# Performance work log

Hardware: AMD Instinct MI355X
Metric: run time of the kernel (lower is better)

Reference implementation:

```python
import jax, jax.numpy as jnp
import numpy as np

T, B, D, O = 2048, 32, 512, 512


def setup_inputs() -> dict:
    key = jax.random.key(0)
    ks = jax.random.split(key, 12)
    s = 0.02
    return {
        "word": jax.random.normal(ks[0], (T, B, D), dtype=jnp.float32),
        "Wf": jax.random.normal(ks[1], (D, D), dtype=jnp.float32) * s,
        "bf": jax.random.normal(ks[2], (D,), dtype=jnp.float32) * s,
        "Wi": jax.random.normal(ks[3], (D, D), dtype=jnp.float32) * s,
        "bi": jax.random.normal(ks[4], (D,), dtype=jnp.float32) * s,
        "Wz": jax.random.normal(ks[5], (D, D), dtype=jnp.float32) * s,
        "bz": jax.random.normal(ks[6], (D,), dtype=jnp.float32) * s,
        "Wo": jax.random.normal(ks[7], (D, D), dtype=jnp.float32) * s,
        "bo": jax.random.normal(ks[8], (D,), dtype=jnp.float32) * s,
        "Wy": jax.random.normal(ks[9], (O, D), dtype=jnp.float32) * s,
        "by": jax.random.normal(ks[10], (O,), dtype=jnp.float32) * s,
    }


def reference(word, Wf, bf, Wi, bi, Wz, bz, Wo, bo, Wy, by):
    # Faithful to the original buggy module:
    #  - forward discards the updated cell state, so c == 0 every step and
    #    the zf gate (wf) never affects the output.
    #  - z and zo reuse wi(hidden) instead of wz/wo(hidden).
    #  - the same Linear is applied to letter and hidden, so bias is doubled
    #    in zi (and zf).
    Bsz, Dd = word.shape[1], word.shape[2]

    def step(h, x):  # h: [B, D], x: [B, D]
        hWi = h @ Wi.T                                  # reused by zi, z, zo
        zi = jax.nn.sigmoid(x @ Wi.T + hWi + 2.0 * bi)
        z = jax.nn.sigmoid(x @ Wz.T + bz + hWi + bi)
        zo = jax.nn.sigmoid(x @ Wo.T + bo + hWi + bi)
        c = zi * z                                      # zf * 0 + zi * z
        h_new = zo * jnp.tanh(c)
        return h_new, None

    h0 = jnp.zeros((Bsz, Dd), dtype=word.dtype)
    h_final, _ = jax.lax.scan(step, h0, word)
    # original computes wy(hidden) every step but only returns the last one
    output = h_final @ Wy.T + by                        # [B, O]
    return output
```

## Files before the change

kernel.cpp:

```cpp
#include <hip/hip_runtime.h>

typedef unsigned int u32;
typedef unsigned short u16;
typedef unsigned long long u64;
typedef _Float16 f16;
typedef f16 f16x2 __attribute__((ext_vector_type(2)));

__device__ __forceinline__ float fdot2(u32 a, u32 b, float c) {
#if __has_builtin(__builtin_amdgcn_fdot2)
    return __builtin_amdgcn_fdot2(__builtin_bit_cast(f16x2, a),
                                  __builtin_bit_cast(f16x2, b), c, false);
#else
    f16x2 av = __builtin_bit_cast(f16x2, a), bv = __builtin_bit_cast(f16x2, b);
    c += (float)av[0] * (float)bv[0];
    c += (float)av[1] * (float)bv[1];
    return c;
#endif
}

__device__ __forceinline__ u32 pack2h(float a, float b) {
    f16x2 h; h[0] = (f16)a; h[1] = (f16)b;
    return __builtin_bit_cast(u32, h);
}
__device__ __forceinline__ float h2f(u16 x) { return (float)__builtin_bit_cast(f16, x); }
__device__ __forceinline__ u16 f2h(float x) { f16 h = (f16)x; return __builtin_bit_cast(u16, h); }

__device__ __forceinline__ float fexp(float x) {
#if __has_builtin(__builtin_amdgcn_exp2f)
    return __builtin_amdgcn_exp2f(x * 1.44269504088896f);
#else
    return __expf(x);
#endif
}
__device__ __forceinline__ float frcp(float x) {
#if __has_builtin(__builtin_amdgcn_rcpf)
    return __builtin_amdgcn_rcpf(x);
#else
    return 1.0f / x;
#endif
}
__device__ __forceinline__ float fsigmoid(float x) { return frcp(1.0f + fexp(-x)); }
__device__ __forceinline__ float ftanh_pos(float x) { return 1.0f - 2.0f * frcp(fexp(2.0f * x) + 1.0f); }

__global__ __launch_bounds__(256) void k0_pack(const float* __restrict__ Wi,
                                               const float* __restrict__ Wy,
                                               u32* __restrict__ WpkT,
                                               u32* __restrict__ Wypk) {
    const int bx = blockIdx.x, tid = threadIdx.x;
    if (bx < 512) {
        const float2 v = *(const float2*)(Wi + (size_t)bx * 512 + 2 * tid);
        WpkT[(size_t)bx * 256 + tid] = pack2h(v.x, v.y);
    } else {
        const int p = bx - 512;
        #pragma unroll
        for (int r = 0; r < 2; ++r) {
            const int d = tid + 256 * r;
            Wypk[(size_t)p * 512 + d] =
                pack2h(Wy[(size_t)d * 512 + 2 * p], Wy[(size_t)d * 512 + 2 * p + 1]);
        }
    }
}

__global__ __launch_bounds__(256) void k1_gates(
    const float* __restrict__ word,
    const float* __restrict__ Wi, const float* __restrict__ Wz, const float* __restrict__ Wo,
    const float* __restrict__ bi, const float* __restrict__ bz, const float* __restrict__ bo,
    u16* __restrict__ Xi, u16* __restrict__ Xz, u16* __restrict__ Xo)
{
    __shared__ uint4 ws2v[3][128][4];
    __shared__ u32 xs2[2][16][36];

    const int tid = threadIdx.x;
    const int d_l = tid & 63;
    const int bq  = tid >> 6;
    const int t0  = blockIdx.x * 2;
    const int d0  = blockIdx.y * 128;

    const float* Wg[3] = {Wi, Wz, Wo};

    float acc[2][2][8][3];
    #pragma unroll
    for (int tt = 0; tt < 2; ++tt)
        #pragma unroll
        for (int db = 0; db < 2; ++db)
            #pragma unroll
            for (int j = 0; j < 8; ++j)
                #pragma unroll
                for (int g = 0; g < 3; ++g) acc[tt][db][j][g] = 0.0f;

    for (int k0c = 0; k0c < 512; k0c += 32) {
        {
            const int p = tid & 15, bg = tid >> 4;
            #pragma unroll
            for (int tt = 0; tt < 2; ++tt)
                #pragma unroll
                for (int j = 0; j < 2; ++j) {
                    const int bb = bg * 2 + j;
                    const float2 v = *(const float2*)(word + (((size_t)(t0 + tt) * 32 + bb) * 512 + k0c + 2 * p));
                    xs2[tt][p][bb] = pack2h(v.x, v.y);
                }
        }
        {
            #pragma unroll
            for (int cc = 0; cc < 6; ++cc) {
                const int c = tid + 256 * cc;
                const int g = c >> 9, r = c & 511, pg = r >> 7, i = r & 127;
                const float* src = Wg[g] + (size_t)(d0 + i) * 512 + k0c + 8 * pg;
                const float4 v0 = ((const float4*)src)[0];
                const float4 v1 = ((const float4*)src)[1];
                uint4 cell;
                cell.x = pack2h(v0.x, v0.y); cell.y = pack2h(v0.z, v0.w);
                cell.z = pack2h(v1.x, v1.y); cell.w = pack2h(v1.z, v1.w);
                ws2v[g][i][(pg + (i >> 2)) & 3] = cell;
            }
        }
        __syncthreads();
        #pragma unroll
        for (int pg = 0; pg < 4; ++pg) {
            uint4 wc[3][2];
            #pragma unroll
            for (int g = 0; g < 3; ++g)
                #pragma unroll
                for (int db = 0; db < 2; ++db) {
                    const int d = d_l + 64 * db;
                    wc[g][db] = ws2v[g][d][(pg + (d >> 2)) & 3];
                }
            #pragma unroll
            for (int p = 0; p < 4; ++p) {
                const int pair = 4 * pg + p;
                u32 x2[2][8];
                #pragma unroll
                for (int tt = 0; tt < 2; ++tt) {
                    const uint4* xr = (const uint4*)&xs2[tt][pair][bq * 8];
                    uint4 xa = xr[0], xb = xr[1];
                    x2[tt][0] = xa.x; x2[tt][1] = xa.y; x2[tt][2] = xa.z; x2[tt][3] = xa.w;
                    x2[tt][4] = xb.x; x2[tt][5] = xb.y; x2[tt][6] = xb.z; x2[tt][7] = xb.w;
                }
                u32 w[3][2];
                #pragma unroll
                for (int g = 0; g < 3; ++g)
                    #pragma unroll
                    for (int db = 0; db < 2; ++db) {
                        const uint4 v = wc[g][db];
                        w[g][db] = (p == 0) ? v.x : (p == 1) ? v.y : (p == 2) ? v.z : v.w;
                    }
                #pragma unroll
                for (int tt = 0; tt < 2; ++tt)
                    #pragma unroll
                    for (int db = 0; db < 2; ++db)
                        #pragma unroll
                        for (int j = 0; j < 8; ++j)
                            #pragma unroll
                            for (int g = 0; g < 3; ++g)
                                acc[tt][db][j][g] = fdot2(x2[tt][j], w[g][db], acc[tt][db][j][g]);
            }
        }
        __syncthreads();
    }

    #pragma unroll
    for (int db = 0; db < 2; ++db) {
        const int d = d0 + 64 * db + d_l;
        const float b0 = 2.0f * bi[d];
        const float b1 = bz[d] + bi[d];
        const float b2 = bo[d] + bi[d];
        #pragma unroll
        for (int tt = 0; tt < 2; ++tt)
            #pragma unroll
            for (int j = 0; j < 8; ++j) {
                const size_t o = ((size_t)(t0 + tt) * 32 + (bq * 8 + j)) * 512 + d;
                Xi[o] = f2h(acc[tt][db][j][0] + b0);
                Xz[o] = f2h(acc[tt][db][j][1] + b1);
                Xo[o] = f2h(acc[tt][db][j][2] + b2);
            }
    }
}

__global__ __launch_bounds__(512, 1) void k2_recur(
    const u16* __restrict__ Xi, const u16* __restrict__ Xz, const u16* __restrict__ Xo,
    const u32* __restrict__ WpkT, const u32* __restrict__ Wypk,
    u64* __restrict__ exch,
    const float* __restrict__ by, float* __restrict__ out)
{
    __shared__ alignas(16) u16 hb[2][256];
    __shared__ alignas(16) u16 hfull[512];

    const int bid  = blockIdx.x;
    const int b    = bid >> 1;
    const int half = bid & 1;
    const int tid  = threadIdx.x;

    const uint4* WpkT4 = (const uint4*)WpkT;
    uint4 w[32];
    #pragma unroll
    for (int i = 0; i < 32; ++i) w[i] = WpkT4[(size_t)tid * 64 + half * 32 + i];

    if (tid < 256) hb[0][tid] = (u16)0;
    __syncthreads();

    u64* eo = exch + ((size_t)(b * 2 + half) * 2) * 512 + tid;
    const u64* ei = exch + ((size_t)(b * 2 + (half ^ 1)) * 2) * 512 + tid;

    const int ownhalf = ((tid >> 8) == half);
    const int hloc = tid & 255;

    u16 xi_c = Xi[(size_t)b * 512 + tid];
    u16 xz_c = Xz[(size_t)b * 512 + tid];
    u16 xo_c = Xo[(size_t)b * 512 + tid];

    float hn = 0.0f;
    for (int t = 0; t < 2048; ++t) {
        const int par = t & 1;
        const int tn = (t + 1) & 2047;
        const size_t xb = ((size_t)tn * 32 + b) * 512 + tid;
        const u16 xi_n = Xi[xb], xz_n = Xz[xb], xo_n = Xo[xb];

        const uint4* hv = (const uint4*)&hb[par][0];
        float a0 = 0.f, a1 = 0.f, a2 = 0.f, a3 = 0.f;
        #pragma unroll
        for (int i = 0; i < 32; ++i) {
            const uint4 hc = hv[i];
            a0 = fdot2(hc.x, w[i].x, a0);
            a1 = fdot2(hc.y, w[i].y, a1);
            a2 = fdot2(hc.z, w[i].z, a2);
            a3 = fdot2(hc.w, w[i].w, a3);
        }
        const float p = (a0 + a1) + (a2 + a3);

        const u64 msg = ((u64)(u32)(t + 1) << 32) | (u64)__builtin_bit_cast(u32, p);
        __hip_atomic_store(eo + (size_t)par * 512, msg,
                           __ATOMIC_RELAXED, __HIP_MEMORY_SCOPE_AGENT);
        u64 m;
        do {
            m = __hip_atomic_load(ei + (size_t)par * 512,
                                  __ATOMIC_RELAXED, __HIP_MEMORY_SCOPE_AGENT);
        } while ((u32)(m >> 32) != (u32)(t + 1));
        const float v = p + __builtin_bit_cast(float, (u32)m);

        const float zi = fsigmoid(h2f(xi_c) + v);
        const float z  = fsigmoid(h2f(xz_c) + v);
        const float zo = fsigmoid(h2f(xo_c) + v);
        hn = zo * ftanh_pos(zi * z);

        if (ownhalf) hb[par ^ 1][hloc] = f2h(hn);
        __syncthreads();

        xi_c = xi_n; xz_c = xz_n; xo_c = xo_n;
    }

    hfull[tid] = f2h(hn);
    __syncthreads();
    {
        const uint4* hv = (const uint4*)&hfull[0];
        float e0 = 0.f, e1 = 0.f, e2 = 0.f, e3 = 0.f;
        #pragma unroll 8
        for (int i = 0; i < 64; ++i) {
            const uint4 hc = hv[i];
            e0 = fdot2(hc.x, Wypk[(size_t)(4 * i + 0) * 512 + tid], e0);
            e1 = fdot2(hc.y, Wypk[(size_t)(4 * i + 1) * 512 + tid], e1);
            e2 = fdot2(hc.z, Wypk[(size_t)(4 * i + 2) * 512 + tid], e2);
            e3 = fdot2(hc.w, Wypk[(size_t)(4 * i + 3) * 512 + tid], e3);
        }
        out[(size_t)b * 512 + tid] = (e0 + e1) + (e2 + e3) + by[tid];
    }
}

extern "C" void kernel_launch(void* const* d_in, const int* in_sizes, int n_in,
                              void* d_out, int out_size, void* d_ws, size_t ws_size,
                              hipStream_t stream) {
    const float* word = (const float*)d_in[0];
    const float* Wi = (const float*)d_in[3];
    const float* bi = (const float*)d_in[4];
    const float* Wz = (const float*)d_in[5];
    const float* bz = (const float*)d_in[6];
    const float* Wo = (const float*)d_in[7];
    const float* bo = (const float*)d_in[8];
    const float* Wy = (const float*)d_in[9];
    const float* by = (const float*)d_in[10];
    float* out = (float*)d_out;

    char* ws = (char*)d_ws;
    const size_t XN = (size_t)2048 * 32 * 512 * sizeof(u16);
    u16* Xi = (u16*)(ws);
    u16* Xz = (u16*)(ws + XN);
    u16* Xo = (u16*)(ws + 2 * XN);
    u32* WpkT = (u32*)(ws + 3 * XN);
    u32* Wypk = (u32*)(ws + 3 * XN + (size_t)524288);
    u64* exch = (u64*)(ws + 3 * XN + (size_t)2 * 524288);

    k0_pack<<<768, 256, 0, stream>>>(Wi, Wy, WpkT, Wypk);

    dim3 g1(1024, 4);
    k1_gates<<<g1, 256, 0, stream>>>(word, Wi, Wz, Wo, bi, bz, bo, Xi, Xz, Xo);

    k2_recur<<<64, 512, 0, stream>>>(Xi, Xz, Xo, WpkT, Wypk, exch, by, out);
}
```

Before: 4.449 ms.

## Exchange partial sums via dual L2/agent channels and remap block pairing

```diff
diff --git a/kernel.cpp b/kernel.cpp
--- a/kernel.cpp
+++ b/kernel.cpp
@@ -41,6 +41,16 @@
 }
 __device__ __forceinline__ float fsigmoid(float x) { return frcp(1.0f + fexp(-x)); }
 __device__ __forceinline__ float ftanh_pos(float x) { return 1.0f - 2.0f * frcp(fexp(2.0f * x) + 1.0f); }
+
+__device__ __forceinline__ u64 load_l2(const u64* p) {
+    u64 v;
+    asm volatile("global_load_dwordx2 %0, %1, off sc0\n\ts_waitcnt vmcnt(0)"
+                 : "=v"(v) : "v"(p) : "memory");
+    return v;
+}
+__device__ __forceinline__ void store_l2(u64* p, u64 v) {
+    asm volatile("global_store_dwordx2 %0, %1, off sc0" :: "v"(p), "v"(v) : "memory");
+}
 
 __global__ __launch_bounds__(256) void k0_pack(const float* __restrict__ Wi,
                                                const float* __restrict__ Wy,
@@ -176,30 +186,38 @@
     }
 }
 
-__global__ __launch_bounds__(512, 1) void k2_recur(
+__global__ __launch_bounds__(512, 2) void k2_recur(
     const u16* __restrict__ Xi, const u16* __restrict__ Xz, const u16* __restrict__ Xo,
     const u32* __restrict__ WpkT, const u32* __restrict__ Wypk,
-    u64* __restrict__ exch,
+    u64* __restrict__ exchF, u64* __restrict__ exchS,
     const float* __restrict__ by, float* __restrict__ out)
 {
     __shared__ alignas(16) u16 hb[2][256];
     __shared__ alignas(16) u16 hfull[512];
 
     const int bid  = blockIdx.x;
-    const int b    = bid >> 1;
-    const int half = bid & 1;
+    const int half = (bid >> 3) & 1;
+    const int b    = (bid & 7) | ((bid >> 4) << 3);
     const int tid  = threadIdx.x;
 
     const uint4* WpkT4 = (const uint4*)WpkT;
-    uint4 w[32];
+    u32 wq[128];
     #pragma unroll
-    for (int i = 0; i < 32; ++i) w[i] = WpkT4[(size_t)tid * 64 + half * 32 + i];
+    for (int i = 0; i < 32; ++i) {
+        const uint4 v = WpkT4[(size_t)tid * 64 + half * 32 + i];
+        wq[4 * i + 0] = v.x; wq[4 * i + 1] = v.y;
+        wq[4 * i + 2] = v.z; wq[4 * i + 3] = v.w;
+    }
+    #pragma unroll
+    for (int i = 0; i < 128; ++i) asm volatile("" : "+v"(wq[i]));
 
     if (tid < 256) hb[0][tid] = (u16)0;
     __syncthreads();
 
-    u64* eo = exch + ((size_t)(b * 2 + half) * 2) * 512 + tid;
-    const u64* ei = exch + ((size_t)(b * 2 + (half ^ 1)) * 2) * 512 + tid;
+    const size_t me  = (size_t)(b * 2 + half) * 2 * 512 + tid;
+    const size_t pa  = (size_t)(b * 2 + (half ^ 1)) * 2 * 512 + tid;
+    u64* eoF = exchF + me;  u64* eoS = exchS + me;
+    const u64* eiF = exchF + pa;  const u64* eiS = exchS + pa;
 
     const int ownhalf = ((tid >> 8) == half);
     const int hloc = tid & 255;
@@ -220,21 +238,27 @@
         #pragma unroll
         for (int i = 0; i < 32; ++i) {
             const uint4 hc = hv[i];
-            a0 = fdot2(hc.x, w[i].x, a0);
-            a1 = fdot2(hc.y, w[i].y, a1);
-            a2 = fdot2(hc.z, w[i].z, a2);
-            a3 = fdot2(hc.w, w[i].w, a3);
+            a0 = fdot2(hc.x, wq[4 * i + 0], a0);
+            a1 = fdot2(hc.y, wq[4 * i + 1], a1);
+            a2 = fdot2(hc.z, wq[4 * i + 2], a2);
+            a3 = fdot2(hc.w, wq[4 * i + 3], a3);
         }
         const float p = (a0 + a1) + (a2 + a3);
 
-        const u64 msg = ((u64)(u32)(t + 1) << 32) | (u64)__builtin_bit_cast(u32, p);
-        __hip_atomic_store(eo + (size_t)par * 512, msg,
+        const u32 tag = (u32)(t + 1);
+        const u64 msg = ((u64)tag << 32) | (u64)__builtin_bit_cast(u32, p);
+        store_l2(eoF + (size_t)par * 512, msg);
+        __hip_atomic_store(eoS + (size_t)par * 512, msg,
                            __ATOMIC_RELAXED, __HIP_MEMORY_SCOPE_AGENT);
+
         u64 m;
-        do {
-            m = __hip_atomic_load(ei + (size_t)par * 512,
+        for (;;) {
+            m = load_l2(eiF + (size_t)par * 512);
+            if ((u32)(m >> 32) == tag) break;
+            m = __hip_atomic_load(eiS + (size_t)par * 512,
                                   __ATOMIC_RELAXED, __HIP_MEMORY_SCOPE_AGENT);
-        } while ((u32)(m >> 32) != (u32)(t + 1));
+            if ((u32)(m >> 32) == tag) break;
+        }
         const float v = p + __builtin_bit_cast(float, (u32)m);
 
         const float zi = fsigmoid(h2f(xi_c) + v);
@@ -284,14 +308,15 @@
     u16* Xi = (u16*)(ws);
     u16* Xz = (u16*)(ws + XN);
     u16* Xo = (u16*)(ws + 2 * XN);
-    u32* WpkT = (u32*)(ws + 3 * XN);
-    u32* Wypk = (u32*)(ws + 3 * XN + (size_t)524288);
-    u64* exch = (u64*)(ws + 3 * XN + (size_t)2 * 524288);
+    u32* WpkT  = (u32*)(ws + 3 * XN);
+    u32* Wypk  = (u32*)(ws + 3 * XN + (size_t)524288);
+    u64* exchF = (u64*)(ws + 3 * XN + (size_t)2 * 524288);
+    u64* exchS = (u64*)(ws + 3 * XN + (size_t)3 * 524288);
 
     k0_pack<<<768, 256, 0, stream>>>(Wi, Wy, WpkT, Wypk);
 
     dim3 g1(1024, 4);
     k1_gates<<<g1, 256, 0, stream>>>(word, Wi, Wz, Wo, bi, bz, bo, Xi, Xz, Xo);
 
-    k2_recur<<<64, 512, 0, stream>>>(Xi, Xz, Xo, WpkT, Wypk, exch, by, out);
-}
+    k2_recur<<<64, 512, 0, stream>>>(Xi, Xz, Xo, WpkT, Wypk, exchF, exchS, by, out);
+}
```

Result: faster. 4.266 ms (-4.1%).
